# Kernel tuning notes

Measured on AMD Instinct MI355X. Metric: run time of the kernel, lower is better.

The kernel has to match this reference:

```python
import jax, jax.numpy as jnp
import numpy as np

NB = 5          # LC kernel size (odd -> L_out == L with pad = NB//2)
S = 8           # num_sparse_LC segments
N_LEVELS = 4
K_DENSE = 3
K_LC = 3
SQ = np.float32(np.sqrt(0.5))


def haar_dec(x):
    # level-1 haar wavedec, periodization mode; x: (..., L), L even
    x0, x1 = x[..., 0::2], x[..., 1::2]
    return (x0 + x1) * SQ, (x0 - x1) * SQ  # (cA, cD)


def haar_rec(cA, cD):
    # inverse of haar_dec
    x0 = (cA + cD) * SQ
    x1 = (cA - cD) * SQ
    return jnp.stack([x0, x1], axis=-1).reshape(cA.shape[:-1] + (-1,))


def lc_apply(x, w, b):
    # cheapPartiallyUnsharedConv1d. x: (B,d,k,2,L); w: (d,k,o=2,i=2,S,NB); b: (d,k,2,S)
    L = x.shape[-1]
    p = NB // 2
    xp = jnp.pad(x, ((0, 0),) * 4 + ((p, p),))
    idx = jnp.arange(L)[:, None] + jnp.arange(NB)[None, :]      # (L, NB)
    patches = xp[..., idx]                                      # (B,d,k,2,L,NB)
    # per-segment weights: floor(L/S) repeats per segment, remainder -> last segment
    R = L // S
    seg = jnp.clip(jnp.arange(L) // R, 0, S - 1)                # (L,)
    wf = w[:, :, :, :, seg, :]                                  # (d,k,o,i,L,NB)
    bf = b[:, :, :, seg]                                        # (d,k,o,L)
    return jnp.einsum('dkoilf,bdkilf->bdkol', wf, patches) + bf


def lin_deriv(ts, ys, t):
    # derivative of linear interpolation of ys over knots ts, evaluated at t
    # ts: (T,); ys: (B,T,D); t: (T,) -> (B,T,D)
    i = jnp.clip(jnp.searchsorted(ts, t, side='right') - 1, 0, ts.shape[0] - 2)
    return (ys[:, i + 1, :] - ys[:, i, :]) / (ts[i + 1] - ts[i])[None, :, None]


def setup_inputs() -> dict:
    key = jax.random.key(0)
    ks = jax.random.split(key, 8)
    B, L, D, d, k = 16, 2048, 64, 32, 16
    dn = L >> N_LEVELS  # 128 == dense_dim
    seq = jax.random.normal(ks[0], (B, L, D), jnp.float32)
    coeffs = jax.random.normal(ks[1], (B, L, D), jnp.float32)
    time_step = jnp.arange(L, dtype=jnp.float32)
    time = jnp.arange(L, dtype=jnp.float32)
    Wg = jax.random.normal(ks[2], (D, d), jnp.float32) * (2.0 / D) ** 0.5
    Wh = jax.random.normal(ks[3], (d, D * k), jnp.float32) * (2.0 / d) ** 0.5
    dense_W = jax.random.normal(ks[4], (K_DENSE, d, k, dn, dn), jnp.float32) * (2.0 / dn) ** 0.5
    lc_w = jax.random.normal(ks[5], (N_LEVELS, K_LC, d, k, 2, 2, S, NB), jnp.float32) * (2.0 / (2 * NB)) ** 0.5
    lc_b = jax.random.uniform(ks[6], (N_LEVELS, K_LC, d, k, 2, S), jnp.float32)
    Wrev = jax.random.normal(ks[7], (d, D), jnp.float32) * (2.0 / d) ** 0.5
    return dict(seq=seq, coeffs=coeffs, time=time, time_step=time_step,
                Wg=Wg, Wh=Wh, dense_W=dense_W, lc_w=lc_w, lc_b=lc_b, Wrev=Wrev)


def reference(seq, coeffs, time, time_step, Wg, Wh, dense_W, lc_w, lc_b, Wrev):
    B, L, D = seq.shape
    d = Wg.shape[1]
    k = Wh.shape[1] // D
    der = lin_deriv(time_step, coeffs, time)                    # (B,L,D) == der_X.squeeze(-1)
    z = jax.nn.relu(seq @ Wg)                                   # (B,L,d)
    h = jax.nn.relu(z @ Wh).reshape(B, L, D, k)                 # (B,L,D,k)
    v = jnp.einsum('blDk,blD->bkl', h, der)                     # (B,k,L)

    # analysis: n_levels of level-1 haar wavedec
    ca = v
    details, approxs = [], []
    for _ in range(N_LEVELS):
        ca, cd = haar_dec(ca)
        details.append(cd)
        approxs.append(ca)

    # coarsest approx -> per-(d,k) dense stack
    cur = jnp.tile(approxs[-1][:, None, :, :], (1, d, 1, 1))    # (B,d,k,dn)
    for j in range(K_DENSE):
        cur = jnp.einsum('dktq,bdkq->bdkt', dense_W[j], cur)

    # synthesis with locally-connected refinements
    for l in reversed(range(N_LEVELS)):
        chi = jnp.tile(jnp.stack([details[l], approxs[l]], axis=2)[:, None],
                       (1, d, 1, 1, 1))                          # (B,d,k,2,Ll)
        for j in range(K_LC):
            chi = jax.nn.relu(lc_apply(chi, lc_w[l, j], lc_b[l, j]))
        # shape_correction is identity: lengths match exactly with haar/pow2
        X = chi.at[:, :, :, 1, :].add(cur)                       # add approx on channel 1
        cur = haar_rec(X[:, :, :, 1, :], X[:, :, :, 0, :])       # (B,d,k,2*Ll)

    out = jnp.sum(cur, axis=2)                                   # (B,d,L)
    U = jnp.transpose(out, (0, 2, 1)) @ Wrev                     # (B,L,D_out)
    return U
```

## Files before the change

kernel.cpp:

```cpp
#include <hip/hip_runtime.h>

#define SQC 0.70710678118654752f

typedef __attribute__((ext_vector_type(8))) short bf16x8;
typedef __attribute__((ext_vector_type(4))) float f32x4;

__device__ __forceinline__ unsigned short bf16_rne(float x) {
  unsigned int u = __float_as_uint(x);
  u += 0x7FFFu + ((u >> 16) & 1u);
  return (unsigned short)(u >> 16);
}

__global__ __launch_bounds__(256) void k_prep_all(const float* __restrict__ Wh,
                                                  unsigned short* __restrict__ WhT,
                                                  const float* __restrict__ lcw,
                                                  const float* __restrict__ lcb,
                                                  float* __restrict__ re) {
  int bid = blockIdx.x;
  if (bid < 128) {
    int i = bid * 256 + threadIdx.x;
    int n = i >> 5, dd = i & 31;
    WhT[i] = bf16_rne(Wh[dd * 1024 + n]);
    return;
  }
  int g = (bid - 128) * 256 + threadIdx.x;
  int l = g / 294912;
  int r1 = g - l * 294912;
  int dk = r1 / 576;
  int i = r1 - dk * 576;
  int j = i / 192;
  int r = i - j * 192;
  int sg = r / 24;
  int t = r - sg * 24;
  float val = 0.f;
  if (t < 20) {
    int oi = t / 5, f = t - oi * 5;
    val = lcw[((size_t)(l * 3 + j) * 512 + dk) * 160 + (oi * 8 + sg) * 5 + f];
  } else if (t < 22) {
    val = lcb[((size_t)(l * 3 + j) * 512 + dk) * 16 + (t - 20) * 8 + sg];
  }
  re[g] = val;
}

__global__ __launch_bounds__(256) void k_z(const float* __restrict__ seq,
                                           const float* __restrict__ Wg,
                                           unsigned short* __restrict__ zout) {
  int t = (blockIdx.x >> 2) * 256 + threadIdx.x;
  int dq = blockIdx.x & 3;
  const float4* srow = (const float4*)(seq + (size_t)t * 64);
  float acc[8];
#pragma unroll
  for (int i = 0; i < 8; ++i) acc[i] = 0.f;
#pragma unroll 4
  for (int D4 = 0; D4 < 16; ++D4) {
    float4 s4 = srow[D4];
    const float* sp = (const float*)&s4;
#pragma unroll
    for (int q = 0; q < 4; ++q) {
      float s = sp[q];
      int D = D4 * 4 + q;
      const float* wr = Wg + D * 32 + dq * 8;
#pragma unroll
      for (int d = 0; d < 8; ++d) acc[d] = fmaf(s, wr[d], acc[d]);
    }
  }
  uint4 o;
  unsigned int* op = (unsigned int*)&o;
#pragma unroll
  for (int i = 0; i < 4; ++i) {
    unsigned int lo = bf16_rne(fmaxf(acc[2 * i], 0.f));
    unsigned int hi = bf16_rne(fmaxf(acc[2 * i + 1], 0.f));
    op[i] = lo | (hi << 16);
  }
  *(uint4*)(zout + (size_t)t * 32 + dq * 8) = o;
}

__global__ __launch_bounds__(256) void k_v(const unsigned short* __restrict__ zb_g,
                                           const float* __restrict__ coeffs,
                                           const unsigned short* __restrict__ WhT,
                                           float* __restrict__ v) {
  __shared__ unsigned short zs[64][40];
  __shared__ float ders[64][68];
  __shared__ float vout[16][68];
  const int tid = threadIdx.x;
  const int b = blockIdx.x >> 5;
  const int lblk = (blockIdx.x & 31) * 64;
  const unsigned int* zrow_g =
      (const unsigned int*)(zb_g + ((size_t)b * 2048 + lblk) * 32);
  for (int i = tid; i < 1024; i += 256) {
    int r = i >> 4, c2 = i & 15;
    *(unsigned int*)&zs[r][c2 * 2] = zrow_g[i];
  }
  for (int i = tid; i < 4096; i += 256) {
    int r = i >> 6, D = i & 63;
    int ii = min(lblk + r, 2046);
    const float* c0 = coeffs + ((size_t)b * 2048 + ii) * 64 + D;
    ders[r][D] = c0[64] - c0[0];
  }
  __syncthreads();
  const int lane = tid & 63;
  const int wv = tid >> 6;
  const int col = lane & 15, quad = lane >> 4;
  bf16x8 afrag = *(bf16x8*)&zs[wv * 16 + col][quad * 8];
  f32x4 vacc = {0.f, 0.f, 0.f, 0.f};
  const unsigned short* bptr = WhT + col * 32 + quad * 8;
  const int lrow0 = wv * 16 + quad * 4;
#pragma unroll 4
  for (int t = 0; t < 64; ++t) {
    bf16x8 bfrag = *(const bf16x8*)(bptr + t * 512);
    f32x4 c = {0.f, 0.f, 0.f, 0.f};
    c = __builtin_amdgcn_mfma_f32_16x16x32_bf16(afrag, bfrag, c, 0, 0, 0);
#pragma unroll
    for (int r = 0; r < 4; ++r)
      vacc[r] = fmaf(fmaxf(c[r], 0.f), ders[lrow0 + r][t], vacc[r]);
  }
#pragma unroll
  for (int r = 0; r < 4; ++r) vout[col][lrow0 + r] = vacc[r];
  __syncthreads();
  for (int i = tid; i < 1024; i += 256) {
    int kk = i >> 6, ll = i & 63;
    v[((size_t)b * 16 + kk) * 2048 + lblk + ll] = vout[kk][ll];
  }
}

__global__ __launch_bounds__(64) void k_haar(const float* __restrict__ v,
                                             float* __restrict__ wdet,
                                             float* __restrict__ wapp,
                                             float* __restrict__ a0T) {
  const int bk = blockIdx.x;
  const int L = threadIdx.x;
  const float* src = v + (size_t)bk * 2048 + L * 32;
  float x[32];
#pragma unroll
  for (int j = 0; j < 8; ++j) *(float4*)&x[4 * j] = ((const float4*)src)[j];
  const size_t base = (size_t)bk * 1920;
  float ca0[16], cd0[16];
#pragma unroll
  for (int i = 0; i < 16; ++i) {
    ca0[i] = (x[2 * i] + x[2 * i + 1]) * SQC;
    cd0[i] = (x[2 * i] - x[2 * i + 1]) * SQC;
  }
  {
    float* wd = wdet + base + L * 16;
    float* wa = wapp + base + L * 16;
#pragma unroll
    for (int j = 0; j < 4; ++j) {
      *(float4*)(wd + 4 * j) = *(float4*)&cd0[4 * j];
      *(float4*)(wa + 4 * j) = *(float4*)&ca0[4 * j];
    }
  }
  float ca1[8], cd1[8];
#pragma unroll
  for (int i = 0; i < 8; ++i) {
    ca1[i] = (ca0[2 * i] + ca0[2 * i + 1]) * SQC;
    cd1[i] = (ca0[2 * i] - ca0[2 * i + 1]) * SQC;
  }
  {
    float* wd = wdet + base + 1024 + L * 8;
    float* wa = wapp + base + 1024 + L * 8;
#pragma unroll
    for (int j = 0; j < 2; ++j) {
      *(float4*)(wd + 4 * j) = *(float4*)&cd1[4 * j];
      *(float4*)(wa + 4 * j) = *(float4*)&ca1[4 * j];
    }
  }
  float ca2[4], cd2[4];
#pragma unroll
  for (int i = 0; i < 4; ++i) {
    ca2[i] = (ca1[2 * i] + ca1[2 * i + 1]) * SQC;
    cd2[i] = (ca1[2 * i] - ca1[2 * i + 1]) * SQC;
  }
  *(float4*)(wdet + base + 1536 + L * 4) = *(float4*)&cd2[0];
  *(float4*)(wapp + base + 1536 + L * 4) = *(float4*)&ca2[0];
  float ca3[2], cd3[2];
#pragma unroll
  for (int i = 0; i < 2; ++i) {
    ca3[i] = (ca2[2 * i] + ca2[2 * i + 1]) * SQC;
    cd3[i] = (ca2[2 * i] - ca2[2 * i + 1]) * SQC;
  }
  *(float2*)(wdet + base + 1792 + L * 2) = *(float2*)&cd3[0];
  *(float2*)(wapp + base + 1792 + L * 2) = *(float2*)&ca3[0];
  const int k = bk & 15, bb = bk >> 4;
  a0T[((size_t)k * 128 + 2 * L) * 16 + bb] = ca3[0];
  a0T[((size_t)k * 128 + 2 * L + 1) * 16 + bb] = ca3[1];
}

__global__ __launch_bounds__(256) void k_dense3(const float* __restrict__ dW,
                                                const float* __restrict__ a0T,
                                                float* __restrict__ curd) {
  __shared__ float bufA[128 * 20];
  __shared__ float bufB[128 * 20];
  const int tid = threadIdx.x;
  const int dk = blockIdx.x;
  const int d = dk >> 4, k = dk & 15;
  {
    const float* src = a0T + (size_t)k * 2048;
    for (int i = tid; i < 2048; i += 256) {
      int q = i >> 4, b = i & 15;
      bufA[q * 20 + b] = src[i];
    }
  }
  const int t = tid & 127;
  const int bh = (tid >> 7) << 3;
  float acc[8];
  float* bin = bufA;
  float* bout = bufB;
#pragma unroll 1
  for (int j = 0; j < 3; ++j) {
    __syncthreads();
    const float* Wt = dW + ((size_t)j * 512 + dk) * 16384 + (size_t)t * 128;
#pragma unroll
    for (int i = 0; i < 8; ++i) acc[i] = 0.f;
#pragma unroll 4
    for (int q4 = 0; q4 < 32; ++q4) {
      float4 wv4 = ((const float4*)Wt)[q4];
      const float* wp = (const float*)&wv4;
#pragma unroll
      for (int qq = 0; qq < 4; ++qq) {
        int q = q4 * 4 + qq;
        float w = wp[qq];
        const float* ar = bin + q * 20 + bh;
        float4 a0 = *(const float4*)(ar);
        float4 a1 = *(const float4*)(ar + 4);
        acc[0] = fmaf(w, a0.x, acc[0]); acc[1] = fmaf(w, a0.y, acc[1]);
        acc[2] = fmaf(w, a0.z, acc[2]); acc[3] = fmaf(w, a0.w, acc[3]);
        acc[4] = fmaf(w, a1.x, acc[4]); acc[5] = fmaf(w, a1.y, acc[5]);
        acc[6] = fmaf(w, a1.z, acc[6]); acc[7] = fmaf(w, a1.w, acc[7]);
      }
    }
    if (j < 2) {
      float* orow = bout + t * 20 + bh;
      *(float4*)orow = make_float4(acc[0], acc[1], acc[2], acc[3]);
      *(float4*)(orow + 4) = make_float4(acc[4], acc[5], acc[6], acc[7]);
      float* tmp = bin; bin = bout; bout = tmp;
    }
  }
#pragma unroll
  for (int i = 0; i < 8; ++i) {
    int b = bh + i;
    curd[(((size_t)b * 32 + d) * 16 + k) * 128 + t] = acc[i];
  }
}

__device__ __forceinline__ void loadw24(float (&wl)[24], const float* p) {
#pragma unroll
  for (int i = 0; i < 6; ++i) *(float4*)&wl[4 * i] = *(const float4*)(p + 4 * i);
}

template <int P>
__device__ __forceinline__ void conv_inplace(int lane, const float (&wl)[24],
                                             float (&x0)[P], float (&x1)[P]) {
  float l00 = __shfl_up(x0[P - 2], 1), l01 = __shfl_up(x0[P - 1], 1);
  float l10 = __shfl_up(x1[P - 2], 1), l11 = __shfl_up(x1[P - 1], 1);
  float r00 = __shfl_down(x0[0], 1), r01 = __shfl_down(x0[1], 1);
  float r10 = __shfl_down(x1[0], 1), r11 = __shfl_down(x1[1], 1);
  if (lane == 0) { l00 = 0.f; l01 = 0.f; l10 = 0.f; l11 = 0.f; }
  if (lane == 63) { r00 = 0.f; r01 = 0.f; r10 = 0.f; r11 = 0.f; }
  float a0 = l00, b0 = l01, a1 = l10, b1 = l11;
#pragma unroll
  for (int i = 0; i < P; ++i) {
    float c0 = x0[i], c1 = x1[i];
    float d0 = (i + 1 < P) ? x0[i + 1] : r00;
    float d1 = (i + 1 < P) ? x1[i + 1] : r10;
    float e0 = (i + 2 < P) ? x0[i + 2] : ((i + 2 == P) ? r00 : r01);
    float e1 = (i + 2 < P) ? x1[i + 2] : ((i + 2 == P) ? r10 : r11);
    float o0 = wl[20], o1 = wl[21];
    o0 = fmaf(wl[0], a0, o0); o0 = fmaf(wl[1], b0, o0); o0 = fmaf(wl[2], c0, o0);
    o0 = fmaf(wl[3], d0, o0); o0 = fmaf(wl[4], e0, o0);
    o0 = fmaf(wl[5], a1, o0); o0 = fmaf(wl[6], b1, o0); o0 = fmaf(wl[7], c1, o0);
    o0 = fmaf(wl[8], d1, o0); o0 = fmaf(wl[9], e1, o0);
    o1 = fmaf(wl[10], a0, o1); o1 = fmaf(wl[11], b0, o1); o1 = fmaf(wl[12], c0, o1);
    o1 = fmaf(wl[13], d0, o1); o1 = fmaf(wl[14], e0, o1);
    o1 = fmaf(wl[15], a1, o1); o1 = fmaf(wl[16], b1, o1); o1 = fmaf(wl[17], c1, o1);
    o1 = fmaf(wl[18], d1, o1); o1 = fmaf(wl[19], e1, o1);
    a0 = b0; b0 = c0; a1 = b1; b1 = c1;
    x0[i] = fmaxf(o0, 0.f);
    x1[i] = fmaxf(o1, 0.f);
  }
}

template <int P>
__device__ __forceinline__ void conv3(int lane, const float* wb, int seg,
                                      float (&x0)[P], float (&x1)[P]) {
  float wl[24];
  loadw24(wl, wb + (0 * 8 + seg) * 24);
  conv_inplace<P>(lane, wl, x0, x1);
  loadw24(wl, wb + (1 * 8 + seg) * 24);
  conv_inplace<P>(lane, wl, x0, x1);
  loadw24(wl, wb + (2 * 8 + seg) * 24);
  conv_inplace<P>(lane, wl, x0, x1);
}

template <int P>
__device__ __forceinline__ void haar_rec_reg(const float (&x0)[P], const float (&x1)[P],
                                             const float (&cur)[P], float (&nxt)[2 * P]) {
#pragma unroll
  for (int i = 0; i < P; ++i) {
    float X1 = x1[i] + cur[i], X0 = x0[i];
    nxt[2 * i] = (X1 + X0) * SQC;
    nxt[2 * i + 1] = (X1 - X0) * SQC;
  }
}

template <int P>
__device__ __forceinline__ void load_chi(const float* __restrict__ wdet,
                                         const float* __restrict__ wapp,
                                         size_t off, float (&x0)[P], float (&x1)[P]) {
#pragma unroll
  for (int i = 0; i < P; i += 2) {
    *(float2*)&x0[i] = *(const float2*)(wdet + off + i);
    *(float2*)&x1[i] = *(const float2*)(wapp + off + i);
  }
}

__global__ __launch_bounds__(256, 2) void k_lc(const float* __restrict__ wdet,
                                               const float* __restrict__ wapp,
                                               const float* __restrict__ curd,
                                               const float* __restrict__ lcw_re,
                                               float* __restrict__ osum01,
                                               float* __restrict__ osum23) {
  __shared__ float wbuf[4][584];
  __shared__ float accb[2][2112];
  const int tid = threadIdx.x;
  const int lane = tid & 63;
  const int wv = tid >> 6;
  const int kg = blockIdx.x & 3;
  const int d = (blockIdx.x >> 2) & 31;
  const int b = blockIdx.x >> 7;
  const int k = kg * 4 + wv;
  const int bk = b * 16 + k;
  const int dk = d * 16 + k;
  const int seg = lane >> 3;
  float* wb = wbuf[wv];

  auto stage_w = [&](int l) {
    const float4* src = (const float4*)(lcw_re + ((size_t)(l * 512) + dk) * 576);
    float4* dst = (float4*)wb;
#pragma unroll
    for (int ii = 0; ii < 3; ++ii) {
      int idx = lane + 64 * ii;
      if (idx < 144) dst[idx] = src[idx];
    }
  };

  float cur4[4];
  {
    float x0[2], x1[2], c3[2];
    stage_w(3);
    load_chi<2>(wdet, wapp, (size_t)bk * 1920 + 1792 + lane * 2, x0, x1);
    *(float2*)&c3[0] = *(const float2*)(curd + (((size_t)b * 32 + d) * 16 + k) * 128 + lane * 2);
    conv3<2>(lane, wb, seg, x0, x1);
    haar_rec_reg<2>(x0, x1, c3, cur4);
  }
  float cur8[8];
  {
    float x0[4], x1[4];
    stage_w(2);
    load_chi<4>(wdet, wapp, (size_t)bk * 1920 + 1536 + lane * 4, x0, x1);
    conv3<4>(lane, wb, seg, x0, x1);
    haar_rec_reg<4>(x0, x1, cur4, cur8);
  }
  float cur16[16];
  {
    float x0[8], x1[8];
    stage_w(1);
    load_chi<8>(wdet, wapp, (size_t)bk * 1920 + 1024 + lane * 8, x0, x1);
    conv3<8>(lane, wb, seg, x0, x1);
    haar_rec_reg<8>(x0, x1, cur8, cur16);
  }
  {
    float x0[16], x1[16];
    stage_w(0);
    load_chi<16>(wdet, wapp, (size_t)bk * 1920 + lane * 16, x0, x1);
    conv3<16>(lane, wb, seg, x0, x1);
    float* arow = &accb[wv & 1][lane * 33];
    if (wv >= 2) {
#pragma unroll
      for (int i = 0; i < 16; ++i) {
        float X1 = x1[i] + cur16[i], X0 = x0[i];
        arow[2 * i] = (X1 + X0) * SQC;
        arow[2 * i + 1] = (X1 - X0) * SQC;
      }
    }
    __syncthreads();
    if (wv < 2) {
#pragma unroll
      for (int i = 0; i < 16; ++i) {
        float X1 = x1[i] + cur16[i], X0 = x0[i];
        arow[2 * i] += (X1 + X0) * SQC;
        arow[2 * i + 1] += (X1 - X0) * SQC;
      }
    }
  }
  __syncthreads();
  float* obase = (kg < 2) ? osum01 : osum23;
  float* orow = obase + ((size_t)(kg & 1) * 512 + (size_t)b * 32 + d) * 2048;
#pragma unroll
  for (int r = 0; r < 8; ++r) {
    int p = r * 256 + tid;
    int L = p >> 5, J = p & 31;
    int a = L * 33 + J;
    orow[p] = accb[0][a] + accb[1][a];
  }
}

__global__ __launch_bounds__(256) void k_final(const float* __restrict__ osum01,
                                               const float* __restrict__ osum23,
                                               const float* __restrict__ Wrev,
                                               float* __restrict__ U) {
  int t = (blockIdx.x >> 2) * 256 + threadIdx.x;
  int Dq = blockIdx.x & 3;
  int b = t >> 11, l = t & 2047;
  float acc[16];
#pragma unroll
  for (int i = 0; i < 16; ++i) acc[i] = 0.f;
  for (int dd = 0; dd < 32; ++dd) {
    size_t off = ((size_t)b * 32 + dd) * 2048 + l;
    float x = osum01[off] + osum01[off + 1048576] +
              osum23[off] + osum23[off + 1048576];
    const float* wr = Wrev + dd * 64 + Dq * 16;
#pragma unroll
    for (int j = 0; j < 16; ++j) acc[j] = fmaf(x, wr[j], acc[j]);
  }
  float* o = U + (size_t)t * 64 + Dq * 16;
#pragma unroll
  for (int i = 0; i < 4; ++i)
    *(float4*)(o + 4 * i) =
        make_float4(acc[4 * i], acc[4 * i + 1], acc[4 * i + 2], acc[4 * i + 3]);
}

extern "C" void kernel_launch(void* const* d_in, const int* in_sizes, int n_in,
                              void* d_out, int out_size, void* d_ws, size_t ws_size,
                              hipStream_t stream) {
  const float* seq    = (const float*)d_in[0];
  const float* coeffs = (const float*)d_in[1];
  const float* Wg   = (const float*)d_in[4];
  const float* Wh   = (const float*)d_in[5];
  const float* dW   = (const float*)d_in[6];
  const float* lcw  = (const float*)d_in[7];
  const float* lcb  = (const float*)d_in[8];
  const float* Wrev = (const float*)d_in[9];
  float* out = (float*)d_out;

  float* w      = (float*)d_ws;
  unsigned short* zb16 = (unsigned short*)(w + 0);
  float* v      = w + 1048576;
  float* a0T    = w + 1572864;
  unsigned short* WhT = (unsigned short*)(w + 1572864 + 16384);
  float* lcw_re = w + 1605632;
  float* curd   = w + 3702784;
  float* osum01 = w + 4751360;
  float* wdet   = w + 6848512;
  float* wapp   = w + 7340032;
  float* osum23 = w + 7831552;

  k_prep_all<<<4736, 256, 0, stream>>>(Wh, WhT, lcw, lcb, lcw_re);
  k_z<<<512, 256, 0, stream>>>(seq, Wg, zb16);
  k_v<<<512, 256, 0, stream>>>(zb16, coeffs, WhT, v);
  k_haar<<<256, 64, 0, stream>>>(v, wdet, wapp, a0T);
  k_dense3<<<512, 256, 0, stream>>>(dW, a0T, curd);
  k_lc<<<2048, 256, 0, stream>>>(wdet, wapp, curd, lcw_re, osum01, osum23);
  k_final<<<512, 256, 0, stream>>>(osum01, osum23, Wrev, out);
}
```

Before: 256.7 us.

## Software-pipeline LC weight staging and chi loads across levels in k_lc

Double-buffers each wave's shared weight buffer and issues global loads for the next level's weights and chi inputs before computing the current level. Register staging is split into issue and commit steps so memory latency can overlap the conv and haar math. Also widens chi loads to float4 for the larger levels. The cost is more registers (all levels' inputs are live at once) and more LDS, which may lower occupancy under launch_bounds(256,2).

```diff
diff --git a/kernel.cpp b/kernel.cpp
--- a/kernel.cpp
+++ b/kernel.cpp
@@ -306,10 +306,18 @@
 __device__ __forceinline__ void load_chi(const float* __restrict__ wdet,
                                          const float* __restrict__ wapp,
                                          size_t off, float (&x0)[P], float (&x1)[P]) {
-#pragma unroll
-  for (int i = 0; i < P; i += 2) {
-    *(float2*)&x0[i] = *(const float2*)(wdet + off + i);
-    *(float2*)&x1[i] = *(const float2*)(wapp + off + i);
+  if constexpr (P >= 4) {
+#pragma unroll
+    for (int i = 0; i < P; i += 4) {
+      *(float4*)&x0[i] = *(const float4*)(wdet + off + i);
+      *(float4*)&x1[i] = *(const float4*)(wapp + off + i);
+    }
+  } else {
+#pragma unroll
+    for (int i = 0; i < P; i += 2) {
+      *(float2*)&x0[i] = *(const float2*)(wdet + off + i);
+      *(float2*)&x1[i] = *(const float2*)(wapp + off + i);
+    }
   }
 }
 
@@ -319,7 +327,7 @@
                                                const float* __restrict__ lcw_re,
                                                float* __restrict__ osum01,
                                                float* __restrict__ osum23) {
-  __shared__ float wbuf[4][584];
+  __shared__ float wbuf[4][2][584];
   __shared__ float accb[2][2112];
   const int tid = threadIdx.x;
   const int lane = tid & 63;
@@ -331,53 +339,64 @@
   const int bk = b * 16 + k;
   const int dk = d * 16 + k;
   const int seg = lane >> 3;
-  float* wb = wbuf[wv];
-
-  auto stage_w = [&](int l) {
+  const size_t base = (size_t)bk * 1920;
+
+  struct StReg { float4 a, b, c; };
+  auto stage_issue = [&](int l) {
     const float4* src = (const float4*)(lcw_re + ((size_t)(l * 512) + dk) * 576);
-    float4* dst = (float4*)wb;
-#pragma unroll
-    for (int ii = 0; ii < 3; ++ii) {
-      int idx = lane + 64 * ii;
-      if (idx < 144) dst[idx] = src[idx];
-    }
+    StReg r;
+    r.a = src[lane];
+    r.b = src[lane + 64];
+    if (lane < 16) r.c = src[lane + 128];
+    return r;
   };
+  auto stage_commit = [&](const StReg& r, int slot) {
+    float4* dst = (float4*)wbuf[wv][slot];
+    dst[lane] = r.a;
+    dst[lane + 64] = r.b;
+    if (lane < 16) dst[lane + 128] = r.c;
+  };
+
+  StReg r3 = stage_issue(3);
+  StReg r2 = stage_issue(2);
+  float c3x0[2], c3x1[2], c3[2];
+  load_chi<2>(wdet, wapp, base + 1792 + lane * 2, c3x0, c3x1);
+  *(float2*)&c3[0] =
+      *(const float2*)(curd + (((size_t)b * 32 + d) * 16 + k) * 128 + lane * 2);
+  float c2x0[4], c2x1[4];
+  load_chi<4>(wdet, wapp, base + 1536 + lane * 4, c2x0, c2x1);
+  stage_commit(r3, 0);
 
   float cur4[4];
+  conv3<2>(lane, wbuf[wv][0], seg, c3x0, c3x1);
+  haar_rec_reg<2>(c3x0, c3x1, c3, cur4);
+
+  StReg r1 = stage_issue(1);
+  float c1x0[8], c1x1[8];
+  load_chi<8>(wdet, wapp, base + 1024 + lane * 8, c1x0, c1x1);
+  stage_commit(r2, 1);
+
+  float cur8[8];
+  conv3<4>(lane, wbuf[wv][1], seg, c2x0, c2x1);
+  haar_rec_reg<4>(c2x0, c2x1, cur4, cur8);
+
+  StReg r0 = stage_issue(0);
+  float c0x0[16], c0x1[16];
+  load_chi<16>(wdet, wapp, base + lane * 16, c0x0, c0x1);
+  stage_commit(r1, 0);
+
+  float cur16[16];
+  conv3<8>(lane, wbuf[wv][0], seg, c1x0, c1x1);
+  haar_rec_reg<8>(c1x0, c1x1, cur8, cur16);
+  stage_commit(r0, 1);
+
   {
-    float x0[2], x1[2], c3[2];
-    stage_w(3);
-    load_chi<2>(wdet, wapp, (size_t)bk * 1920 + 1792 + lane * 2, x0, x1);
-    *(float2*)&c3[0] = *(const float2*)(curd + (((size_t)b * 32 + d) * 16 + k) * 128 + lane * 2);
-    conv3<2>(lane, wb, seg, x0, x1);
-    haar_rec_reg<2>(x0, x1, c3, cur4);
-  }
-  float cur8[8];
-  {
-    float x0[4], x1[4];
-    stage_w(2);
-    load_chi<4>(wdet, wapp, (size_t)bk * 1920 + 1536 + lane * 4, x0, x1);
-    conv3<4>(lane, wb, seg, x0, x1);
-    haar_rec_reg<4>(x0, x1, cur4, cur8);
-  }
-  float cur16[16];
-  {
-    float x0[8], x1[8];
-    stage_w(1);
-    load_chi<8>(wdet, wapp, (size_t)bk * 1920 + 1024 + lane * 8, x0, x1);
-    conv3<8>(lane, wb, seg, x0, x1);
-    haar_rec_reg<8>(x0, x1, cur8, cur16);
-  }
-  {
-    float x0[16], x1[16];
-    stage_w(0);
-    load_chi<16>(wdet, wapp, (size_t)bk * 1920 + lane * 16, x0, x1);
-    conv3<16>(lane, wb, seg, x0, x1);
+    conv3<16>(lane, wbuf[wv][1], seg, c0x0, c0x1);
     float* arow = &accb[wv & 1][lane * 33];
     if (wv >= 2) {
 #pragma unroll
       for (int i = 0; i < 16; ++i) {
-        float X1 = x1[i] + cur16[i], X0 = x0[i];
+        float X1 = c0x1[i] + cur16[i], X0 = c0x0[i];
         arow[2 * i] = (X1 + X0) * SQC;
         arow[2 * i + 1] = (X1 - X0) * SQC;
       }
@@ -386,7 +405,7 @@
     if (wv < 2) {
 #pragma unroll
       for (int i = 0; i < 16; ++i) {
-        float X1 = x1[i] + cur16[i], X0 = x0[i];
+        float X1 = c0x1[i] + cur16[i], X0 = c0x0[i];
         arow[2 * i] += (X1 + X0) * SQC;
         arow[2 * i + 1] += (X1 - X0) * SQC;
       }
```

Measured after the change: 258.5 us. About the same (+0.7%).

## Fuse z and v kernels and process two batches per LC block

Applied to the files above, without the earlier changes.

Merges the z projection into the v kernel so z is computed straight into shared memory, removing one launch and a global round trip through a bf16 buffer. The LC kernel now handles two batch elements per block, sharing the staged weights and interleaving two independent FMA chains for more instruction-level parallelism, with half as many blocks. Chi loads are widened to float4. The cost is much higher register pressure under launch_bounds(256,2), a doubled shared accumulator, and fewer blocks, all of which can lower occupancy or cause spills.

```diff
diff --git a/kernel.cpp b/kernel.cpp
--- a/kernel.cpp
+++ b/kernel.cpp
@@ -42,54 +42,46 @@
   re[g] = val;
 }
 
-__global__ __launch_bounds__(256) void k_z(const float* __restrict__ seq,
-                                           const float* __restrict__ Wg,
-                                           unsigned short* __restrict__ zout) {
-  int t = (blockIdx.x >> 2) * 256 + threadIdx.x;
-  int dq = blockIdx.x & 3;
-  const float4* srow = (const float4*)(seq + (size_t)t * 64);
-  float acc[8];
-#pragma unroll
-  for (int i = 0; i < 8; ++i) acc[i] = 0.f;
-#pragma unroll 4
-  for (int D4 = 0; D4 < 16; ++D4) {
-    float4 s4 = srow[D4];
-    const float* sp = (const float*)&s4;
-#pragma unroll
-    for (int q = 0; q < 4; ++q) {
-      float s = sp[q];
-      int D = D4 * 4 + q;
-      const float* wr = Wg + D * 32 + dq * 8;
-#pragma unroll
-      for (int d = 0; d < 8; ++d) acc[d] = fmaf(s, wr[d], acc[d]);
-    }
-  }
-  uint4 o;
-  unsigned int* op = (unsigned int*)&o;
-#pragma unroll
-  for (int i = 0; i < 4; ++i) {
-    unsigned int lo = bf16_rne(fmaxf(acc[2 * i], 0.f));
-    unsigned int hi = bf16_rne(fmaxf(acc[2 * i + 1], 0.f));
-    op[i] = lo | (hi << 16);
-  }
-  *(uint4*)(zout + (size_t)t * 32 + dq * 8) = o;
-}
-
-__global__ __launch_bounds__(256) void k_v(const unsigned short* __restrict__ zb_g,
-                                           const float* __restrict__ coeffs,
-                                           const unsigned short* __restrict__ WhT,
-                                           float* __restrict__ v) {
+__global__ __launch_bounds__(256) void k_zv(const float* __restrict__ seq,
+                                            const float* __restrict__ Wg,
+                                            const float* __restrict__ coeffs,
+                                            const unsigned short* __restrict__ WhT,
+                                            float* __restrict__ v) {
   __shared__ unsigned short zs[64][40];
   __shared__ float ders[64][68];
   __shared__ float vout[16][68];
   const int tid = threadIdx.x;
   const int b = blockIdx.x >> 5;
   const int lblk = (blockIdx.x & 31) * 64;
-  const unsigned int* zrow_g =
-      (const unsigned int*)(zb_g + ((size_t)b * 2048 + lblk) * 32);
-  for (int i = tid; i < 1024; i += 256) {
-    int r = i >> 4, c2 = i & 15;
-    *(unsigned int*)&zs[r][c2 * 2] = zrow_g[i];
+  {
+    const int r = tid >> 2;
+    const int dq = tid & 3;
+    const float4* srow = (const float4*)(seq + ((size_t)b * 2048 + lblk + r) * 64);
+    float acc[8];
+#pragma unroll
+    for (int i = 0; i < 8; ++i) acc[i] = 0.f;
+#pragma unroll 4
+    for (int D4 = 0; D4 < 16; ++D4) {
+      float4 s4 = srow[D4];
+      const float* sp = (const float*)&s4;
+#pragma unroll
+      for (int q = 0; q < 4; ++q) {
+        float s = sp[q];
+        int D = D4 * 4 + q;
+        const float* wr = Wg + D * 32 + dq * 8;
+#pragma unroll
+        for (int dd2 = 0; dd2 < 8; ++dd2) acc[dd2] = fmaf(s, wr[dd2], acc[dd2]);
+      }
+    }
+    uint4 o;
+    unsigned int* op = (unsigned int*)&o;
+#pragma unroll
+    for (int i = 0; i < 4; ++i) {
+      unsigned int lo = bf16_rne(fmaxf(acc[2 * i], 0.f));
+      unsigned int hi = bf16_rne(fmaxf(acc[2 * i + 1], 0.f));
+      op[i] = lo | (hi << 16);
+    }
+    *(uint4*)&zs[r][dq * 8] = o;
   }
   for (int i = tid; i < 4096; i += 256) {
     int r = i >> 6, D = i & 63;
@@ -248,47 +240,78 @@
 }
 
 template <int P>
-__device__ __forceinline__ void conv_inplace(int lane, const float (&wl)[24],
-                                             float (&x0)[P], float (&x1)[P]) {
-  float l00 = __shfl_up(x0[P - 2], 1), l01 = __shfl_up(x0[P - 1], 1);
-  float l10 = __shfl_up(x1[P - 2], 1), l11 = __shfl_up(x1[P - 1], 1);
-  float r00 = __shfl_down(x0[0], 1), r01 = __shfl_down(x0[1], 1);
-  float r10 = __shfl_down(x1[0], 1), r11 = __shfl_down(x1[1], 1);
-  if (lane == 0) { l00 = 0.f; l01 = 0.f; l10 = 0.f; l11 = 0.f; }
-  if (lane == 63) { r00 = 0.f; r01 = 0.f; r10 = 0.f; r11 = 0.f; }
-  float a0 = l00, b0 = l01, a1 = l10, b1 = l11;
+__device__ __forceinline__ void conv_inplace2(int lane, const float (&wl)[24],
+                                              float (&xa0)[P], float (&xa1)[P],
+                                              float (&xb0)[P], float (&xb1)[P]) {
+  float la00 = __shfl_up(xa0[P - 2], 1), la01 = __shfl_up(xa0[P - 1], 1);
+  float la10 = __shfl_up(xa1[P - 2], 1), la11 = __shfl_up(xa1[P - 1], 1);
+  float ra00 = __shfl_down(xa0[0], 1), ra01 = __shfl_down(xa0[1], 1);
+  float ra10 = __shfl_down(xa1[0], 1), ra11 = __shfl_down(xa1[1], 1);
+  float lb00 = __shfl_up(xb0[P - 2], 1), lb01 = __shfl_up(xb0[P - 1], 1);
+  float lb10 = __shfl_up(xb1[P - 2], 1), lb11 = __shfl_up(xb1[P - 1], 1);
+  float rb00 = __shfl_down(xb0[0], 1), rb01 = __shfl_down(xb0[1], 1);
+  float rb10 = __shfl_down(xb1[0], 1), rb11 = __shfl_down(xb1[1], 1);
+  if (lane == 0) {
+    la00 = 0.f; la01 = 0.f; la10 = 0.f; la11 = 0.f;
+    lb00 = 0.f; lb01 = 0.f; lb10 = 0.f; lb11 = 0.f;
+  }
+  if (lane == 63) {
+    ra00 = 0.f; ra01 = 0.f; ra10 = 0.f; ra11 = 0.f;
+    rb00 = 0.f; rb01 = 0.f; rb10 = 0.f; rb11 = 0.f;
+  }
+  float aa0 = la00, ba0 = la01, aa1 = la10, ba1 = la11;
+  float ab0 = lb00, bb0 = lb01, ab1 = lb10, bb1 = lb11;
 #pragma unroll
   for (int i = 0; i < P; ++i) {
-    float c0 = x0[i], c1 = x1[i];
-    float d0 = (i + 1 < P) ? x0[i + 1] : r00;
-    float d1 = (i + 1 < P) ? x1[i + 1] : r10;
-    float e0 = (i + 2 < P) ? x0[i + 2] : ((i + 2 == P) ? r00 : r01);
-    float e1 = (i + 2 < P) ? x1[i + 2] : ((i + 2 == P) ? r10 : r11);
-    float o0 = wl[20], o1 = wl[21];
-    o0 = fmaf(wl[0], a0, o0); o0 = fmaf(wl[1], b0, o0); o0 = fmaf(wl[2], c0, o0);
-    o0 = fmaf(wl[3], d0, o0); o0 = fmaf(wl[4], e0, o0);
-    o0 = fmaf(wl[5], a1, o0); o0 = fmaf(wl[6], b1, o0); o0 = fmaf(wl[7], c1, o0);
-    o0 = fmaf(wl[8], d1, o0); o0 = fmaf(wl[9], e1, o0);
-    o1 = fmaf(wl[10], a0, o1); o1 = fmaf(wl[11], b0, o1); o1 = fmaf(wl[12], c0, o1);
-    o1 = fmaf(wl[13], d0, o1); o1 = fmaf(wl[14], e0, o1);
-    o1 = fmaf(wl[15], a1, o1); o1 = fmaf(wl[16], b1, o1); o1 = fmaf(wl[17], c1, o1);
-    o1 = fmaf(wl[18], d1, o1); o1 = fmaf(wl[19], e1, o1);
-    a0 = b0; b0 = c0; a1 = b1; b1 = c1;
-    x0[i] = fmaxf(o0, 0.f);
-    x1[i] = fmaxf(o1, 0.f);
+    float ca0 = xa0[i], ca1 = xa1[i];
+    float da0 = (i + 1 < P) ? xa0[i + 1] : ra00;
+    float da1 = (i + 1 < P) ? xa1[i + 1] : ra10;
+    float ea0 = (i + 2 < P) ? xa0[i + 2] : ((i + 2 == P) ? ra00 : ra01);
+    float ea1 = (i + 2 < P) ? xa1[i + 2] : ((i + 2 == P) ? ra10 : ra11);
+    float cb0 = xb0[i], cb1 = xb1[i];
+    float db0 = (i + 1 < P) ? xb0[i + 1] : rb00;
+    float db1 = (i + 1 < P) ? xb1[i + 1] : rb10;
+    float eb0 = (i + 2 < P) ? xb0[i + 2] : ((i + 2 == P) ? rb00 : rb01);
+    float eb1 = (i + 2 < P) ? xb1[i + 2] : ((i + 2 == P) ? rb10 : rb11);
+    float oA0 = wl[20], oA1 = wl[21], oB0 = wl[20], oB1 = wl[21];
+    oA0 = fmaf(wl[0], aa0, oA0); oB0 = fmaf(wl[0], ab0, oB0);
+    oA1 = fmaf(wl[10], aa0, oA1); oB1 = fmaf(wl[10], ab0, oB1);
+    oA0 = fmaf(wl[1], ba0, oA0); oB0 = fmaf(wl[1], bb0, oB0);
+    oA1 = fmaf(wl[11], ba0, oA1); oB1 = fmaf(wl[11], bb0, oB1);
+    oA0 = fmaf(wl[2], ca0, oA0); oB0 = fmaf(wl[2], cb0, oB0);
+    oA1 = fmaf(wl[12], ca0, oA1); oB1 = fmaf(wl[12], cb0, oB1);
+    oA0 = fmaf(wl[3], da0, oA0); oB0 = fmaf(wl[3], db0, oB0);
+    oA1 = fmaf(wl[13], da0, oA1); oB1 = fmaf(wl[13], db0, oB1);
+    oA0 = fmaf(wl[4], ea0, oA0); oB0 = fmaf(wl[4], eb0, oB0);
+    oA1 = fmaf(wl[14], ea0, oA1); oB1 = fmaf(wl[14], eb0, oB1);
+    oA0 = fmaf(wl[5], aa1, oA0); oB0 = fmaf(wl[5], ab1, oB0);
+    oA1 = fmaf(wl[15], aa1, oA1); oB1 = fmaf(wl[15], ab1, oB1);
+    oA0 = fmaf(wl[6], ba1, oA0); oB0 = fmaf(wl[6], bb1, oB0);
+    oA1 = fmaf(wl[16], ba1, oA1); oB1 = fmaf(wl[16], bb1, oB1);
+    oA0 = fmaf(wl[7], ca1, oA0); oB0 = fmaf(wl[7], cb1, oB0);
+    oA1 = fmaf(wl[17], ca1, oA1); oB1 = fmaf(wl[17], cb1, oB1);
+    oA0 = fmaf(wl[8], da1, oA0); oB0 = fmaf(wl[8], db1, oB0);
+    oA1 = fmaf(wl[18], da1, oA1); oB1 = fmaf(wl[18], db1, oB1);
+    oA0 = fmaf(wl[9], ea1, oA0); oB0 = fmaf(wl[9], eb1, oB0);
+    oA1 = fmaf(wl[19], ea1, oA1); oB1 = fmaf(wl[19], eb1, oB1);
+    aa0 = ba0; ba0 = ca0; aa1 = ba1; ba1 = ca1;
+    ab0 = bb0; bb0 = cb0; ab1 = bb1; bb1 = cb1;
+    xa0[i] = fmaxf(oA0, 0.f); xa1[i] = fmaxf(oA1, 0.f);
+    xb0[i] = fmaxf(oB0, 0.f); xb1[i] = fmaxf(oB1, 0.f);
   }
 }
 
 template <int P>
-__device__ __forceinline__ void conv3(int lane, const float* wb, int seg,
-                                      float (&x0)[P], float (&x1)[P]) {
+__device__ __forceinline__ void conv3_2(int lane, const float* wb, int seg,
+                                        float (&xa0)[P], float (&xa1)[P],
+                                        float (&xb0)[P], float (&xb1)[P]) {
   float wl[24];
   loadw24(wl, wb + (0 * 8 + seg) * 24);
-  conv_inplace<P>(lane, wl, x0, x1);
+  conv_inplace2<P>(lane, wl, xa0, xa1, xb0, xb1);
   loadw24(wl, wb + (1 * 8 + seg) * 24);
-  conv_inplace<P>(lane, wl, x0, x1);
+  conv_inplace2<P>(lane, wl, xa0, xa1, xb0, xb1);
   loadw24(wl, wb + (2 * 8 + seg) * 24);
-  conv_inplace<P>(lane, wl, x0, x1);
+  conv_inplace2<P>(lane, wl, xa0, xa1, xb0, xb1);
 }
 
 template <int P>
@@ -306,10 +329,18 @@
 __device__ __forceinline__ void load_chi(const float* __restrict__ wdet,
                                          const float* __restrict__ wapp,
                                          size_t off, float (&x0)[P], float (&x1)[P]) {
-#pragma unroll
-  for (int i = 0; i < P; i += 2) {
-    *(float2*)&x0[i] = *(const float2*)(wdet + off + i);
-    *(float2*)&x1[i] = *(const float2*)(wapp + off + i);
+  if constexpr (P >= 4) {
+#pragma unroll
+    for (int i = 0; i < P; i += 4) {
+      *(float4*)&x0[i] = *(const float4*)(wdet + off + i);
+      *(float4*)&x1[i] = *(const float4*)(wapp + off + i);
+    }
+  } else {
+#pragma unroll
+    for (int i = 0; i < P; i += 2) {
+      *(float2*)&x0[i] = *(const float2*)(wdet + off + i);
+      *(float2*)&x1[i] = *(const float2*)(wapp + off + i);
+    }
   }
 }
 
@@ -320,16 +351,18 @@
                                                float* __restrict__ osum01,
                                                float* __restrict__ osum23) {
   __shared__ float wbuf[4][584];
-  __shared__ float accb[2][2112];
+  __shared__ float accb[2][2][2112];
   const int tid = threadIdx.x;
   const int lane = tid & 63;
   const int wv = tid >> 6;
   const int kg = blockIdx.x & 3;
   const int d = (blockIdx.x >> 2) & 31;
-  const int b = blockIdx.x >> 7;
+  const int bp = blockIdx.x >> 7;
   const int k = kg * 4 + wv;
-  const int bk = b * 16 + k;
   const int dk = d * 16 + k;
+  const int b0 = bp * 2, b1 = b0 + 1;
+  const size_t base0 = ((size_t)b0 * 16 + k) * 1920;
+  const size_t base1 = ((size_t)b1 * 16 + k) * 1920;
   const int seg = lane >> 3;
   float* wb = wbuf[wv];
 
@@ -343,64 +376,82 @@
     }
   };
 
-  float cur4[4];
-  {
-    float x0[2], x1[2], c3[2];
+  float cur4a[4], cur4b[4];
+  {
+    float xa0[2], xa1[2], xb0[2], xb1[2], c3a[2], c3b[2];
     stage_w(3);
-    load_chi<2>(wdet, wapp, (size_t)bk * 1920 + 1792 + lane * 2, x0, x1);
-    *(float2*)&c3[0] = *(const float2*)(curd + (((size_t)b * 32 + d) * 16 + k) * 128 + lane * 2);
-    conv3<2>(lane, wb, seg, x0, x1);
-    haar_rec_reg<2>(x0, x1, c3, cur4);
-  }
-  float cur8[8];
-  {
-    float x0[4], x1[4];
+    load_chi<2>(wdet, wapp, base0 + 1792 + lane * 2, xa0, xa1);
+    load_chi<2>(wdet, wapp, base1 + 1792 + lane * 2, xb0, xb1);
+    *(float2*)&c3a[0] =
+        *(const float2*)(curd + (((size_t)b0 * 32 + d) * 16 + k) * 128 + lane * 2);
+    *(float2*)&c3b[0] =
+        *(const float2*)(curd + (((size_t)b1 * 32 + d) * 16 + k) * 128 + lane * 2);
+    conv3_2<2>(lane, wb, seg, xa0, xa1, xb0, xb1);
+    haar_rec_reg<2>(xa0, xa1, c3a, cur4a);
+    haar_rec_reg<2>(xb0, xb1, c3b, cur4b);
+  }
+  float cur8a[8], cur8b[8];
+  {
+    float xa0[4], xa1[4], xb0[4], xb1[4];
     stage_w(2);
-    load_chi<4>(wdet, wapp, (size_t)bk * 1920 + 1536 + lane * 4, x0, x1);
-    conv3<4>(lane, wb, seg, x0, x1);
-    haar_rec_reg<4>(x0, x1, cur4, cur8);
-  }
-  float cur16[16];
-  {
-    float x0[8], x1[8];
+    load_chi<4>(wdet, wapp, base0 + 1536 + lane * 4, xa0, xa1);
+    load_chi<4>(wdet, wapp, base1 + 1536 + lane * 4, xb0, xb1);
+    conv3_2<4>(lane, wb, seg, xa0, xa1, xb0, xb1);
+    haar_rec_reg<4>(xa0, xa1, cur4a, cur8a);
+    haar_rec_reg<4>(xb0, xb1, cur4b, cur8b);
+  }
+  float cur16a[16], cur16b[16];
+  {
+    float xa0[8], xa1[8], xb0[8], xb1[8];
     stage_w(1);
-    load_chi<8>(wdet, wapp, (size_t)bk * 1920 + 1024 + lane * 8, x0, x1);
-    conv3<8>(lane, wb, seg, x0, x1);
-    haar_rec_reg<8>(x0, x1, cur8, cur16);
-  }
-  {
-    float x0[16], x1[16];
+    load_chi<8>(wdet, wapp, base0 + 1024 + lane * 8, xa0, xa1);
+    load_chi<8>(wdet, wapp, base1 + 1024 + lane * 8, xb0, xb1);
+    conv3_2<8>(lane, wb, seg, xa0, xa1, xb0, xb1);
+    haar_rec_reg<8>(xa0, xa1, cur8a, cur16a);
+    haar_rec_reg<8>(xb0, xb1, cur8b, cur16b);
+  }
+  {
+    float xa0[16], xa1[16], xb0[16], xb1[16];
     stage_w(0);
-    load_chi<16>(wdet, wapp, (size_t)bk * 1920 + lane * 16, x0, x1);
-    conv3<16>(lane, wb, seg, x0, x1);
-    float* arow = &accb[wv & 1][lane * 33];
+    load_chi<16>(wdet, wapp, base0 + lane * 16, xa0, xa1);
+    load_chi<16>(wdet, wapp, base1 + lane * 16, xb0, xb1);
+    conv3_2<16>(lane, wb, seg, xa0, xa1, xb0, xb1);
+    float* arowA = &accb[0][wv & 1][lane * 33];
+    float* arowB = &accb[1][wv & 1][lane * 33];
     if (wv >= 2) {
 #pragma unroll
       for (int i = 0; i < 16; ++i) {
-        float X1 = x1[i] + cur16[i], X0 = x0[i];
-        arow[2 * i] = (X1 + X0) * SQC;
-        arow[2 * i + 1] = (X1 - X0) * SQC;
+        float X1a = xa1[i] + cur16a[i], X0a = xa0[i];
+        arowA[2 * i] = (X1a + X0a) * SQC;
+        arowA[2 * i + 1] = (X1a - X0a) * SQC;
+        float X1b = xb1[i] + cur16b[i], X0b = xb0[i];
+        arowB[2 * i] = (X1b + X0b) * SQC;
+        arowB[2 * i + 1] = (X1b - X0b) * SQC;
       }
     }
     __syncthreads();
     if (wv < 2) {
 #pragma unroll
       for (int i = 0; i < 16; ++i) {
-        float X1 = x1[i] + cur16[i], X0 = x0[i];
-        arow[2 * i] += (X1 + X0) * SQC;
-        arow[2 * i + 1] += (X1 - X0) * SQC;
+        float X1a = xa1[i] + cur16a[i], X0a = xa0[i];
+        arowA[2 * i] += (X1a + X0a) * SQC;
+        arowA[2 * i + 1] += (X1a - X0a) * SQC;
+        float X1b = xb1[i] + cur16b[i], X0b = xb0[i];
+        arowB[2 * i] += (X1b + X0b) * SQC;
+        arowB[2 * i + 1] += (X1b - X0b) * SQC;
       }
     }
   }
   __syncthreads();
   float* obase = (kg < 2) ? osum01 : osum23;
-  float* orow = obase + ((size_t)(kg & 1) * 512 + (size_t)b * 32 + d) * 2048;
-#pragma unroll
-  for (int r = 0; r < 8; ++r) {
+#pragma unroll
+  for (int r = 0; r < 16; ++r) {
     int p = r * 256 + tid;
-    int L = p >> 5, J = p & 31;
-    int a = L * 33 + J;
-    orow[p] = accb[0][a] + accb[1][a];
+    int bi = p >> 11, q = p & 2047;
+    int L = q >> 5, J = q & 31;
+    float* orow = obase +
+        ((size_t)(kg & 1) * 512 + (size_t)(bp * 2 + bi) * 32 + d) * 2048;
+    orow[q] = accb[bi][0][L * 33 + J] + accb[bi][1][L * 33 + J];
   }
 }
 
@@ -443,7 +494,6 @@
   float* out = (float*)d_out;
 
   float* w      = (float*)d_ws;
-  unsigned short* zb16 = (unsigned short*)(w + 0);
   float* v      = w + 1048576;
   float* a0T    = w + 1572864;
   unsigned short* WhT = (unsigned short*)(w + 1572864 + 16384);
@@ -455,10 +505,9 @@
   float* osum23 = w + 7831552;
 
   k_prep_all<<<4736, 256, 0, stream>>>(Wh, WhT, lcw, lcb, lcw_re);
-  k_z<<<512, 256, 0, stream>>>(seq, Wg, zb16);
-  k_v<<<512, 256, 0, stream>>>(zb16, coeffs, WhT, v);
+  k_zv<<<512, 256, 0, stream>>>(seq, Wg, coeffs, WhT, v);
   k_haar<<<256, 64, 0, stream>>>(v, wdet, wapp, a0T);
   k_dense3<<<512, 256, 0, stream>>>(dW, a0T, curd);
-  k_lc<<<2048, 256, 0, stream>>>(wdet, wapp, curd, lcw_re, osum01, osum23);
+  k_lc<<<1024, 256, 0, stream>>>(wdet, wapp, curd, lcw_re, osum01, osum23);
   k_final<<<512, 256, 0, stream>>>(osum01, osum23, Wrev, out);
 }
```

Measured after the change: 282.1 us. +9.9%, slower.
